# Performance work log

Hardware: AMD Instinct MI355X
Metric: run time of the kernel (lower is better)

## Reference

```python
import jax, jax.numpy as jnp
jax.config.update("jax_enable_x64", True)
import numpy as np

B = 1_000_000

def _basis_and_weights():
    # 7 Lie-algebra generators of the homography group (4x4), as in the torch module
    E = np.zeros((7, 4, 4), dtype=np.float64)
    E[0, 0, 3] = 1.0   # x translation
    E[1, 1, 3] = 1.0   # y translation
    E[2, 2, 3] = 1.0   # z translation
    E[3, 1, 2] = -1.0; E[3, 2, 1] = 1.0   # yz rotation generator
    E[4, 0, 2] = 1.0;  E[4, 2, 0] = -1.0  # xz rotation generator
    E[5, 0, 1] = -1.0; E[5, 1, 0] = 1.0   # xy rotation generator
    E[6, 0, 0] = 1.0;  E[6, 1, 1] = -1.0  # xy stretch generator
    w = np.ones((7,), dtype=np.float64)   # all *_weight init kwargs = 1.0
    return jnp.asarray(E), jnp.asarray(w)


def setup_inputs() -> dict:
    key = jax.random.key(0)
    lie_vectors = jax.random.normal(key, (B, 7), dtype=jnp.float32)
    return {"lie_vectors": lie_vectors}


def reference(lie_vectors):
    elements, weights = _basis_and_weights()
    # weighted sum of basis elements: (B,7) x (7,4,4) -> (B,4,4), in float64 (dtype_cast_to)
    A = jnp.einsum("bk,kij->bij", lie_vectors.astype(jnp.float64) * weights, elements)
    # batched 4x4 matrix exponential
    T = jax.vmap(jax.scipy.linalg.expm)(A)
    # homogeneous normalization by the (3,3) entry
    T = T / T[:, 3:4, 3:4]
    return T.astype(jnp.float32)  # dtype_out
```

## Files before the change

### kernel.cpp

```cpp
#include <hip/hip_runtime.h>

#define BLOCK 256

__global__ __launch_bounds__(BLOCK) void lie_expm_kernel(
    const float* __restrict__ in, float* __restrict__ out, int B)
{
    __shared__ float sh[BLOCK * 16];
    const int tid = threadIdx.x;
    const long long blockBase = (long long)blockIdx.x * BLOCK;

    {
        int valid = B - (int)blockBase;
        if (valid > BLOCK) valid = BLOCK;
        const int limit = valid * 7;
        const int nf4 = limit >> 2;
        const float4* in4 = (const float4*)(in + blockBase * 7);
        float4* sh4 = (float4*)sh;
        #pragma unroll
        for (int it = 0; it < 2; ++it) {
            const int idx = it * BLOCK + tid;
            if (idx < nf4) sh4[idx] = in4[idx];
        }
        const int remf = limit & 3;
        if (tid < remf) sh[nf4 * 4 + tid] = in[blockBase * 7 + nf4 * 4 + tid];
        #pragma unroll
        for (int it = 0; it < 7; ++it) {
            const int i = it * BLOCK + tid;
            if (i >= limit && i < BLOCK * 7) sh[i] = 0.0f;
        }
    }
    __syncthreads();

    const float v0 = sh[tid * 7 + 0];
    const float v1 = sh[tid * 7 + 1];
    const float v2 = sh[tid * 7 + 2];
    const float v3 = sh[tid * 7 + 3];
    const float v4 = sh[tid * 7 + 4];
    const float v5 = sh[tid * 7 + 5];
    const float v6 = sh[tid * 7 + 6];

    float X[3][4] = {
        {  v6, -v5,  v4, v0 },
        {  v5, -v6, -v3, v1 },
        { -v4,  v3, 0.0f, v2 }
    };

    float n0 = fabsf(X[0][0]) + fabsf(X[0][1]) + fabsf(X[0][2]) + fabsf(X[0][3]);
    float n1 = fabsf(X[1][0]) + fabsf(X[1][1]) + fabsf(X[1][2]) + fabsf(X[1][3]);
    float n2 = fabsf(X[2][0]) + fabsf(X[2][1]) + fabsf(X[2][2]) + fabsf(X[2][3]);
    float nrm = fmaxf(n0, fmaxf(n1, n2));
    #pragma unroll
    for (int off = 32; off >= 1; off >>= 1)
        nrm = fmaxf(nrm, __shfl_xor(nrm, off, 64));
    int e = (int)((__float_as_uint(nrm) >> 23) & 0xFFu) - 126;
    int s = min(max(e + 1, 0), 8);
    s = __builtin_amdgcn_readfirstlane(s);
    const float sc = __uint_as_float((unsigned)(127 - s) << 23);

    #pragma unroll
    for (int i = 0; i < 3; i++)
        #pragma unroll
        for (int c = 0; c < 4; c++)
            X[i][c] *= sc;

    float A2[3][4];
    #pragma unroll
    for (int i = 0; i < 3; i++) {
        #pragma unroll
        for (int c = 0; c < 4; c++) {
            float acc = X[i][0] * X[0][c];
            acc = fmaf(X[i][1], X[1][c], acc);
            acc = fmaf(X[i][2], X[2][c], acc);
            A2[i][c] = acc;
        }
    }

    const float c120 = 1.0f / 120.0f;
    const float c10  = 0.1f;
    float W[3][4];
    #pragma unroll
    for (int i = 0; i < 3; i++)
        #pragma unroll
        for (int c = 0; c < 4; c++)
            W[i][c] = fmaf(A2[i][c], c120, (i == c) ? 0.5f : 0.0f);

    float Nm[3][4], Dm[3][4];
    #pragma unroll
    for (int i = 0; i < 3; i++) {
        #pragma unroll
        for (int c = 0; c < 4; c++) {
            float u = (c == 3) ? 0.5f * X[i][3] : 0.0f;
            u = fmaf(X[i][0], W[0][c], u);
            u = fmaf(X[i][1], W[1][c], u);
            u = fmaf(X[i][2], W[2][c], u);
            float v = fmaf(A2[i][c], c10, (i == c) ? 1.0f : 0.0f);
            Nm[i][c] = v + u;
            Dm[i][c] = v - u;
        }
    }

    const float d00 = Dm[0][0], d01 = Dm[0][1], d02 = Dm[0][2];
    const float d10 = Dm[1][0], d11 = Dm[1][1], d12 = Dm[1][2];
    const float d20 = Dm[2][0], d21 = Dm[2][1], d22 = Dm[2][2];
    const float a00 = fmaf(d11, d22, -d12 * d21);
    const float a01 = fmaf(d02, d21, -d01 * d22);
    const float a02 = fmaf(d01, d12, -d02 * d11);
    const float a10 = fmaf(d12, d20, -d10 * d22);
    const float a11 = fmaf(d00, d22, -d02 * d20);
    const float a12 = fmaf(d02, d10, -d00 * d12);
    const float a20 = fmaf(d10, d21, -d11 * d20);
    const float a21 = fmaf(d01, d20, -d00 * d21);
    const float a22 = fmaf(d00, d11, -d01 * d10);
    float det = d00 * a00 + d01 * a10 + d02 * a20;
    float r = __builtin_amdgcn_rcpf(det);
    r = r * fmaf(-det, r, 2.0f);
    const float i00 = a00 * r, i01 = a01 * r, i02 = a02 * r;
    const float i10 = a10 * r, i11 = a11 * r, i12 = a12 * r;
    const float i20 = a20 * r, i21 = a21 * r, i22 = a22 * r;

    float P[3][4];
    float rhs0 = Nm[0][3] - Dm[0][3], rhs1 = Nm[1][3] - Dm[1][3], rhs2 = Nm[2][3] - Dm[2][3];
    #pragma unroll
    for (int c = 0; c < 3; c++) {
        P[0][c] = i00 * Nm[0][c] + i01 * Nm[1][c] + i02 * Nm[2][c];
        P[1][c] = i10 * Nm[0][c] + i11 * Nm[1][c] + i12 * Nm[2][c];
        P[2][c] = i20 * Nm[0][c] + i21 * Nm[1][c] + i22 * Nm[2][c];
    }
    P[0][3] = i00 * rhs0 + i01 * rhs1 + i02 * rhs2;
    P[1][3] = i10 * rhs0 + i11 * rhs1 + i12 * rhs2;
    P[2][3] = i20 * rhs0 + i21 * rhs1 + i22 * rhs2;

    for (int q = 0; q < s; q++) {
        float T[3][4];
        #pragma unroll
        for (int i = 0; i < 3; i++) {
            #pragma unroll
            for (int c = 0; c < 4; c++) {
                float acc = (c == 3) ? P[i][3] : 0.0f;
                acc = fmaf(P[i][0], P[0][c], acc);
                acc = fmaf(P[i][1], P[1][c], acc);
                acc = fmaf(P[i][2], P[2][c], acc);
                T[i][c] = acc;
            }
        }
        #pragma unroll
        for (int i = 0; i < 3; i++)
            #pragma unroll
            for (int c = 0; c < 4; c++)
                P[i][c] = T[i][c];
    }

    __syncthreads();
    {
        float4* sh4 = (float4*)sh;
        const int rot = (tid >> 1) & 3;
        #pragma unroll
        for (int i = 0; i < 4; i++) {
            const int qp = (i + rot) & 3;
            float4 q;
            if (i < 3) q = make_float4(P[i][0], P[i][1], P[i][2], P[i][3]);
            else       q = make_float4(0.0f, 0.0f, 0.0f, 1.0f);
            sh4[tid * 4 + qp] = q;
        }
    }
    __syncthreads();
    {
        const float4* sh4 = (const float4*)sh;
        float4* out4 = (float4*)(out + blockBase * 16);
        long long vq = ((long long)B - blockBase) * 4;
        const int validquads = (vq > BLOCK * 4) ? (BLOCK * 4) : (int)vq;
        #pragma unroll
        for (int it = 0; it < 4; it++) {
            const int g = it * BLOCK + tid;
            const int row = g >> 2, k = g & 3;
            const float4 val = sh4[(row << 2) | ((k + ((row >> 1) & 3)) & 3)];
            if (g < validquads) out4[g] = val;
        }
    }
}

extern "C" void kernel_launch(void* const* d_in, const int* in_sizes, int n_in,
                              void* d_out, int out_size, void* d_ws, size_t ws_size,
                              hipStream_t stream) {
    const float* in = (const float*)d_in[0];
    float* out = (float*)d_out;
    const int B = in_sizes[0] / 7;
    const int grid = (B + BLOCK - 1) / BLOCK;
    lie_expm_kernel<<<grid, BLOCK, 0, stream>>>(in, out, B);
}
```

Measured before the change: 89.29 us.

## Make expm kernel persistent with register prefetch of the next tile's input

Converts the one-block-per-tile launch into a persistent grid-stride kernel capped at a fixed grid size. Each block prefetches the next tile's input into registers while it computes the current tile, and input and output staging now use separate shared buffers so one barrier per stage is enough. The aim is to hide global load latency and cut block launch overhead. The costs are lower occupancy limits from launch bounds and the extra registers, plus tail loads that are clamped instead of zero-filled.

```diff
diff --git a/kernel.cpp b/kernel.cpp
--- a/kernel.cpp
+++ b/kernel.cpp
@@ -1,180 +1,202 @@
 #include <hip/hip_runtime.h>
 
 #define BLOCK 256
-
-__global__ __launch_bounds__(BLOCK) void lie_expm_kernel(
+#define GRID_BLOCKS 1536
+
+__global__ __launch_bounds__(BLOCK, 6) void lie_expm_kernel(
     const float* __restrict__ in, float* __restrict__ out, int B)
 {
-    __shared__ float sh[BLOCK * 16];
+    __shared__ float shIn[BLOCK * 7];
+    __shared__ float shOut[BLOCK * 16];
     const int tid = threadIdx.x;
-    const long long blockBase = (long long)blockIdx.x * BLOCK;
-
+    const int numTiles = (B + BLOCK - 1) / BLOCK;
+    const long long totF = (long long)B * 7;
+    const long long TOT4 = totF >> 2;
+    const float4* __restrict__ in4 = (const float4*)in;
+
+    int t = blockIdx.x;
+    float4 r0, r1;
     {
-        int valid = B - (int)blockBase;
-        if (valid > BLOCK) valid = BLOCK;
-        const int limit = valid * 7;
-        const int nf4 = limit >> 2;
-        const float4* in4 = (const float4*)(in + blockBase * 7);
-        float4* sh4 = (float4*)sh;
-        #pragma unroll
-        for (int it = 0; it < 2; ++it) {
-            const int idx = it * BLOCK + tid;
-            if (idx < nf4) sh4[idx] = in4[idx];
-        }
-        const int remf = limit & 3;
-        if (tid < remf) sh[nf4 * 4 + tid] = in[blockBase * 7 + nf4 * 4 + tid];
-        #pragma unroll
-        for (int it = 0; it < 7; ++it) {
-            const int i = it * BLOCK + tid;
-            if (i >= limit && i < BLOCK * 7) sh[i] = 0.0f;
-        }
+        const long long base4 = (long long)t * (BLOCK * 7 / 4);
+        long long i0 = base4 + tid;
+        long long i1 = base4 + BLOCK + tid;
+        r0 = in4[i0 < TOT4 ? i0 : TOT4 - 1];
+        r1 = in4[i1 < TOT4 ? i1 : TOT4 - 1];
     }
-    __syncthreads();
-
-    const float v0 = sh[tid * 7 + 0];
-    const float v1 = sh[tid * 7 + 1];
-    const float v2 = sh[tid * 7 + 2];
-    const float v3 = sh[tid * 7 + 3];
-    const float v4 = sh[tid * 7 + 4];
-    const float v5 = sh[tid * 7 + 5];
-    const float v6 = sh[tid * 7 + 6];
-
-    float X[3][4] = {
-        {  v6, -v5,  v4, v0 },
-        {  v5, -v6, -v3, v1 },
-        { -v4,  v3, 0.0f, v2 }
-    };
-
-    float n0 = fabsf(X[0][0]) + fabsf(X[0][1]) + fabsf(X[0][2]) + fabsf(X[0][3]);
-    float n1 = fabsf(X[1][0]) + fabsf(X[1][1]) + fabsf(X[1][2]) + fabsf(X[1][3]);
-    float n2 = fabsf(X[2][0]) + fabsf(X[2][1]) + fabsf(X[2][2]) + fabsf(X[2][3]);
-    float nrm = fmaxf(n0, fmaxf(n1, n2));
-    #pragma unroll
-    for (int off = 32; off >= 1; off >>= 1)
-        nrm = fmaxf(nrm, __shfl_xor(nrm, off, 64));
-    int e = (int)((__float_as_uint(nrm) >> 23) & 0xFFu) - 126;
-    int s = min(max(e + 1, 0), 8);
-    s = __builtin_amdgcn_readfirstlane(s);
-    const float sc = __uint_as_float((unsigned)(127 - s) << 23);
-
-    #pragma unroll
-    for (int i = 0; i < 3; i++)
-        #pragma unroll
-        for (int c = 0; c < 4; c++)
-            X[i][c] *= sc;
-
-    float A2[3][4];
-    #pragma unroll
-    for (int i = 0; i < 3; i++) {
-        #pragma unroll
-        for (int c = 0; c < 4; c++) {
-            float acc = X[i][0] * X[0][c];
-            acc = fmaf(X[i][1], X[1][c], acc);
-            acc = fmaf(X[i][2], X[2][c], acc);
-            A2[i][c] = acc;
-        }
-    }
-
-    const float c120 = 1.0f / 120.0f;
-    const float c10  = 0.1f;
-    float W[3][4];
-    #pragma unroll
-    for (int i = 0; i < 3; i++)
-        #pragma unroll
-        for (int c = 0; c < 4; c++)
-            W[i][c] = fmaf(A2[i][c], c120, (i == c) ? 0.5f : 0.0f);
-
-    float Nm[3][4], Dm[3][4];
-    #pragma unroll
-    for (int i = 0; i < 3; i++) {
-        #pragma unroll
-        for (int c = 0; c < 4; c++) {
-            float u = (c == 3) ? 0.5f * X[i][3] : 0.0f;
-            u = fmaf(X[i][0], W[0][c], u);
-            u = fmaf(X[i][1], W[1][c], u);
-            u = fmaf(X[i][2], W[2][c], u);
-            float v = fmaf(A2[i][c], c10, (i == c) ? 1.0f : 0.0f);
-            Nm[i][c] = v + u;
-            Dm[i][c] = v - u;
-        }
-    }
-
-    const float d00 = Dm[0][0], d01 = Dm[0][1], d02 = Dm[0][2];
-    const float d10 = Dm[1][0], d11 = Dm[1][1], d12 = Dm[1][2];
-    const float d20 = Dm[2][0], d21 = Dm[2][1], d22 = Dm[2][2];
-    const float a00 = fmaf(d11, d22, -d12 * d21);
-    const float a01 = fmaf(d02, d21, -d01 * d22);
-    const float a02 = fmaf(d01, d12, -d02 * d11);
-    const float a10 = fmaf(d12, d20, -d10 * d22);
-    const float a11 = fmaf(d00, d22, -d02 * d20);
-    const float a12 = fmaf(d02, d10, -d00 * d12);
-    const float a20 = fmaf(d10, d21, -d11 * d20);
-    const float a21 = fmaf(d01, d20, -d00 * d21);
-    const float a22 = fmaf(d00, d11, -d01 * d10);
-    float det = d00 * a00 + d01 * a10 + d02 * a20;
-    float r = __builtin_amdgcn_rcpf(det);
-    r = r * fmaf(-det, r, 2.0f);
-    const float i00 = a00 * r, i01 = a01 * r, i02 = a02 * r;
-    const float i10 = a10 * r, i11 = a11 * r, i12 = a12 * r;
-    const float i20 = a20 * r, i21 = a21 * r, i22 = a22 * r;
-
-    float P[3][4];
-    float rhs0 = Nm[0][3] - Dm[0][3], rhs1 = Nm[1][3] - Dm[1][3], rhs2 = Nm[2][3] - Dm[2][3];
-    #pragma unroll
-    for (int c = 0; c < 3; c++) {
-        P[0][c] = i00 * Nm[0][c] + i01 * Nm[1][c] + i02 * Nm[2][c];
-        P[1][c] = i10 * Nm[0][c] + i11 * Nm[1][c] + i12 * Nm[2][c];
-        P[2][c] = i20 * Nm[0][c] + i21 * Nm[1][c] + i22 * Nm[2][c];
-    }
-    P[0][3] = i00 * rhs0 + i01 * rhs1 + i02 * rhs2;
-    P[1][3] = i10 * rhs0 + i11 * rhs1 + i12 * rhs2;
-    P[2][3] = i20 * rhs0 + i21 * rhs1 + i22 * rhs2;
-
-    for (int q = 0; q < s; q++) {
-        float T[3][4];
+
+    for (; t < numTiles; t += GRID_BLOCKS) {
+        const long long tileBase = (long long)t * BLOCK;
+
+        {
+            float4* s4 = (float4*)shIn;
+            s4[tid] = r0;
+            if (tid < BLOCK * 7 / 4 - BLOCK) s4[BLOCK + tid] = r1;
+        }
+        if ((totF & 3LL) && t == numTiles - 1) {
+            const long long firstMissing = TOT4 << 2;
+            const int nmiss = (int)(totF - firstMissing);
+            const int loc = (int)(firstMissing - tileBase * 7);
+            if (tid < nmiss && loc + tid < BLOCK * 7)
+                shIn[loc + tid] = in[firstMissing + tid];
+        }
+        __syncthreads();
+
+        {
+            const int tn = t + GRID_BLOCKS;
+            if (tn < numTiles) {
+                const long long base4 = (long long)tn * (BLOCK * 7 / 4);
+                long long i0 = base4 + tid;
+                long long i1 = base4 + BLOCK + tid;
+                r0 = in4[i0 < TOT4 ? i0 : TOT4 - 1];
+                r1 = in4[i1 < TOT4 ? i1 : TOT4 - 1];
+            }
+        }
+
+        const float v0 = shIn[tid * 7 + 0];
+        const float v1 = shIn[tid * 7 + 1];
+        const float v2 = shIn[tid * 7 + 2];
+        const float v3 = shIn[tid * 7 + 3];
+        const float v4 = shIn[tid * 7 + 4];
+        const float v5 = shIn[tid * 7 + 5];
+        const float v6 = shIn[tid * 7 + 6];
+
+        float X[3][4] = {
+            {  v6, -v5,  v4, v0 },
+            {  v5, -v6, -v3, v1 },
+            { -v4,  v3, 0.0f, v2 }
+        };
+
+        float n0 = fabsf(X[0][0]) + fabsf(X[0][1]) + fabsf(X[0][2]) + fabsf(X[0][3]);
+        float n1 = fabsf(X[1][0]) + fabsf(X[1][1]) + fabsf(X[1][2]) + fabsf(X[1][3]);
+        float n2 = fabsf(X[2][0]) + fabsf(X[2][1]) + fabsf(X[2][2]) + fabsf(X[2][3]);
+        float nrm = fmaxf(n0, fmaxf(n1, n2));
+        #pragma unroll
+        for (int off = 32; off >= 1; off >>= 1)
+            nrm = fmaxf(nrm, __shfl_xor(nrm, off, 64));
+        int e = (int)((__float_as_uint(nrm) >> 23) & 0xFFu) - 126;
+        int s = min(max(e + 1, 0), 8);
+        s = __builtin_amdgcn_readfirstlane(s);
+        const float sc = __uint_as_float((unsigned)(127 - s) << 23);
+
+        #pragma unroll
+        for (int i = 0; i < 3; i++)
+            #pragma unroll
+            for (int c = 0; c < 4; c++)
+                X[i][c] *= sc;
+
+        float A2[3][4];
         #pragma unroll
         for (int i = 0; i < 3; i++) {
             #pragma unroll
             for (int c = 0; c < 4; c++) {
-                float acc = (c == 3) ? P[i][3] : 0.0f;
-                acc = fmaf(P[i][0], P[0][c], acc);
-                acc = fmaf(P[i][1], P[1][c], acc);
-                acc = fmaf(P[i][2], P[2][c], acc);
-                T[i][c] = acc;
-            }
-        }
+                float acc = X[i][0] * X[0][c];
+                acc = fmaf(X[i][1], X[1][c], acc);
+                acc = fmaf(X[i][2], X[2][c], acc);
+                A2[i][c] = acc;
+            }
+        }
+
+        const float c120 = 1.0f / 120.0f;
+        const float c10  = 0.1f;
+        float W[3][4];
         #pragma unroll
         for (int i = 0; i < 3; i++)
             #pragma unroll
             for (int c = 0; c < 4; c++)
-                P[i][c] = T[i][c];
-    }
-
-    __syncthreads();
-    {
-        float4* sh4 = (float4*)sh;
-        const int rot = (tid >> 1) & 3;
-        #pragma unroll
-        for (int i = 0; i < 4; i++) {
-            const int qp = (i + rot) & 3;
-            float4 q;
-            if (i < 3) q = make_float4(P[i][0], P[i][1], P[i][2], P[i][3]);
-            else       q = make_float4(0.0f, 0.0f, 0.0f, 1.0f);
-            sh4[tid * 4 + qp] = q;
-        }
-    }
-    __syncthreads();
-    {
-        const float4* sh4 = (const float4*)sh;
-        float4* out4 = (float4*)(out + blockBase * 16);
-        long long vq = ((long long)B - blockBase) * 4;
-        const int validquads = (vq > BLOCK * 4) ? (BLOCK * 4) : (int)vq;
-        #pragma unroll
-        for (int it = 0; it < 4; it++) {
-            const int g = it * BLOCK + tid;
-            const int row = g >> 2, k = g & 3;
-            const float4 val = sh4[(row << 2) | ((k + ((row >> 1) & 3)) & 3)];
-            if (g < validquads) out4[g] = val;
+                W[i][c] = fmaf(A2[i][c], c120, (i == c) ? 0.5f : 0.0f);
+
+        float Nm[3][4], Dm[3][4];
+        #pragma unroll
+        for (int i = 0; i < 3; i++) {
+            #pragma unroll
+            for (int c = 0; c < 4; c++) {
+                float u = (c == 3) ? 0.5f * X[i][3] : 0.0f;
+                u = fmaf(X[i][0], W[0][c], u);
+                u = fmaf(X[i][1], W[1][c], u);
+                u = fmaf(X[i][2], W[2][c], u);
+                float v = fmaf(A2[i][c], c10, (i == c) ? 1.0f : 0.0f);
+                Nm[i][c] = v + u;
+                Dm[i][c] = v - u;
+            }
+        }
+
+        const float d00 = Dm[0][0], d01 = Dm[0][1], d02 = Dm[0][2];
+        const float d10 = Dm[1][0], d11 = Dm[1][1], d12 = Dm[1][2];
+        const float d20 = Dm[2][0], d21 = Dm[2][1], d22 = Dm[2][2];
+        const float a00 = fmaf(d11, d22, -d12 * d21);
+        const float a01 = fmaf(d02, d21, -d01 * d22);
+        const float a02 = fmaf(d01, d12, -d02 * d11);
+        const float a10 = fmaf(d12, d20, -d10 * d22);
+        const float a11 = fmaf(d00, d22, -d02 * d20);
+        const float a12 = fmaf(d02, d10, -d00 * d12);
+        const float a20 = fmaf(d10, d21, -d11 * d20);
+        const float a21 = fmaf(d01, d20, -d00 * d21);
+        const float a22 = fmaf(d00, d11, -d01 * d10);
+        float det = d00 * a00 + d01 * a10 + d02 * a20;
+        float r = __builtin_amdgcn_rcpf(det);
+        r = r * fmaf(-det, r, 2.0f);
+        const float i00 = a00 * r, i01 = a01 * r, i02 = a02 * r;
+        const float i10 = a10 * r, i11 = a11 * r, i12 = a12 * r;
+        const float i20 = a20 * r, i21 = a21 * r, i22 = a22 * r;
+
+        float P[3][4];
+        float rhs0 = Nm[0][3] - Dm[0][3], rhs1 = Nm[1][3] - Dm[1][3], rhs2 = Nm[2][3] - Dm[2][3];
+        #pragma unroll
+        for (int c = 0; c < 3; c++) {
+            P[0][c] = i00 * Nm[0][c] + i01 * Nm[1][c] + i02 * Nm[2][c];
+            P[1][c] = i10 * Nm[0][c] + i11 * Nm[1][c] + i12 * Nm[2][c];
+            P[2][c] = i20 * Nm[0][c] + i21 * Nm[1][c] + i22 * Nm[2][c];
+        }
+        P[0][3] = i00 * rhs0 + i01 * rhs1 + i02 * rhs2;
+        P[1][3] = i10 * rhs0 + i11 * rhs1 + i12 * rhs2;
+        P[2][3] = i20 * rhs0 + i21 * rhs1 + i22 * rhs2;
+
+        for (int q = 0; q < s; q++) {
+            float T[3][4];
+            #pragma unroll
+            for (int i = 0; i < 3; i++) {
+                #pragma unroll
+                for (int c = 0; c < 4; c++) {
+                    float acc = (c == 3) ? P[i][3] : 0.0f;
+                    acc = fmaf(P[i][0], P[0][c], acc);
+                    acc = fmaf(P[i][1], P[1][c], acc);
+                    acc = fmaf(P[i][2], P[2][c], acc);
+                    T[i][c] = acc;
+                }
+            }
+            #pragma unroll
+            for (int i = 0; i < 3; i++)
+                #pragma unroll
+                for (int c = 0; c < 4; c++)
+                    P[i][c] = T[i][c];
+        }
+
+        {
+            float4* s4 = (float4*)shOut;
+            const int rot = (tid >> 1) & 3;
+            #pragma unroll
+            for (int i = 0; i < 4; i++) {
+                const int qp = (i + rot) & 3;
+                float4 q;
+                if (i < 3) q = make_float4(P[i][0], P[i][1], P[i][2], P[i][3]);
+                else       q = make_float4(0.0f, 0.0f, 0.0f, 1.0f);
+                s4[tid * 4 + qp] = q;
+            }
+        }
+        __syncthreads();
+
+        {
+            const float4* s4 = (const float4*)shOut;
+            float4* out4 = (float4*)(out + tileBase * 16);
+            long long vq = ((long long)B - tileBase) * 4;
+            const int validquads = (vq > BLOCK * 4) ? (BLOCK * 4) : (int)vq;
+            #pragma unroll
+            for (int it = 0; it < 4; it++) {
+                const int g = it * BLOCK + tid;
+                const int row = g >> 2, k = g & 3;
+                const float4 val = s4[(row << 2) | ((k + ((row >> 1) & 3)) & 3)];
+                if (g < validquads) out4[g] = val;
+            }
         }
     }
 }
@@ -185,6 +207,7 @@
     const float* in = (const float*)d_in[0];
     float* out = (float*)d_out;
     const int B = in_sizes[0] / 7;
-    const int grid = (B + BLOCK - 1) / BLOCK;
+    const int numTiles = (B + BLOCK - 1) / BLOCK;
+    const int grid = (numTiles < GRID_BLOCKS) ? numTiles : GRID_BLOCKS;
     lie_expm_kernel<<<grid, BLOCK, 0, stream>>>(in, out, B);
 }
```

After: 99.07 us. 1.11x slower.
